# Optimization experiments

Measured on AMD Instinct MI355X. Metric: run time of the kernel, lower is better.

Reference implementation:

```python
import jax, jax.numpy as jnp
import numpy as np
import math

NQ = 6        # n_qubits_data
NL = 2        # n_layers (active_layers == n_layers)
K = 3         # unfold kernel
C = 64        # channels
SD = 128      # style_dim
B, H, W = 8, 64, 64
PD = C * K * K  # patch_dim = 576


def _apply_1q(psi, U, w):
    # psi: [bsz, 2,2,...,2]; U: [2,2] or [bsz,2,2]
    psi = jnp.moveaxis(psi, 1 + w, -1)
    if U.ndim == 2:
        psi = jnp.einsum('...j,ij->...i', psi, U)
    else:
        psi = jnp.einsum('b...j,bij->b...i', psi, U)
    return jnp.moveaxis(psi, -1, 1 + w)


def _ry_mat(theta):
    c = jnp.cos(theta / 2)
    s = jnp.sin(theta / 2)
    m = jnp.stack([jnp.stack([c, -s], -1), jnp.stack([s, c], -1)], -2)
    return m.astype(jnp.complex64)


def _rz_mat(theta):
    t = theta.astype(jnp.complex64)
    em = jnp.exp(-0.5j * t)
    ep = jnp.exp(0.5j * t)
    z = jnp.zeros_like(em)
    return jnp.stack([jnp.stack([em, z], -1), jnp.stack([z, ep], -1)], -2)


def _u3_mat(theta, phi, lam):
    t = theta.astype(jnp.complex64)
    p = phi.astype(jnp.complex64)
    l = lam.astype(jnp.complex64)
    ct = jnp.cos(t / 2)
    st = jnp.sin(t / 2)
    return jnp.stack([
        jnp.stack([ct, -jnp.exp(1j * l) * st], -1),
        jnp.stack([jnp.exp(1j * p) * st, jnp.exp(1j * (p + l)) * ct], -1)
    ], -2)


def _cnot(psi, c, t):
    c0, c1 = jnp.split(psi, 2, axis=1 + c)
    c1 = jnp.flip(c1, axis=1 + t)
    return jnp.concatenate([c0, c1], axis=1 + c)


def _forward(x, style, data_proj_w, data_proj_b, style_to_data_w, style_to_data_b,
             qcnn_rot_params, measure_params, out_proj_w, out_proj_b,
             res_proj_w, res_proj_b):
    Bx, Cx, Hx, Wx = x.shape
    # nn.Unfold(3, padding=1): [B, C*9, H*W], channel-major then kernel pos
    xp = jnp.pad(x, ((0, 0), (0, 0), (1, 1), (1, 1)))
    pats = jnp.stack([xp[:, :, i:i + Hx, j:j + Wx]
                      for i in range(K) for j in range(K)], axis=2)  # [B,C,9,H,W]
    patches_flat = pats.reshape(Bx, Cx * K * K, Hx * Wx).transpose(0, 2, 1).reshape(-1, Cx * K * K)
    style_flat = jnp.broadcast_to(style[:, None, :], (Bx, Hx * Wx, style.shape[-1])).reshape(-1, style.shape[-1])

    data_angles = jnp.tanh(patches_flat @ data_proj_w.T + data_proj_b) * math.pi   # [bsz, NQ]
    style_angles = jnp.tanh(style_flat @ style_to_data_w.T + style_to_data_b) * math.pi

    bsz = patches_flat.shape[0]
    psi = jnp.zeros((bsz,) + (2,) * NQ, jnp.complex64)
    psi = psi.at[(slice(None),) + (0,) * NQ].set(1.0)

    # hybrid encoding: RY(data + style) per wire (batched angles)
    theta0 = data_angles + style_angles
    for i in range(NQ):
        psi = _apply_1q(psi, _ry_mat(theta0[:, i]), i)

    # HEA layers: per-wire RY/RZ (scalar params) + ring CNOTs
    for l in range(NL):
        for i in range(NQ):
            psi = _apply_1q(psi, _ry_mat(qcnn_rot_params[l, i, 0, 0]), i)
            psi = _apply_1q(psi, _rz_mat(qcnn_rot_params[l, i, 1, 0]), i)
        for i in range(NQ):
            psi = _cnot(psi, i, (i + 1) % NQ)

    # trainable measurement basis (U3 per wire)
    for i in range(NQ):
        psi = _apply_1q(psi, _u3_mat(measure_params[i, 0], measure_params[i, 1], measure_params[i, 2]), i)

    # PauliZ expvals on all wires
    probs = psi.real ** 2 + psi.imag ** 2
    expvals = []
    for i in range(NQ):
        p = jnp.sum(probs, axis=tuple(a for a in range(1, NQ + 1) if a != 1 + i))  # [bsz,2]
        expvals.append(p[:, 0] - p[:, 1])
    quant_out = jnp.stack(expvals, -1)  # [bsz, NQ]

    out_flat = (quant_out @ out_proj_w.T + out_proj_b) + (patches_flat @ res_proj_w.T + res_proj_b)
    return out_flat.reshape(Bx, Hx, Wx, -1).transpose(0, 3, 1, 2)


def setup_inputs() -> dict:
    key = jax.random.key(0)
    ks = jax.random.split(key, 10)
    return {
        'x': jax.random.normal(ks[0], (B, C, H, W), jnp.float32),
        'style': jax.random.normal(ks[1], (B, SD), jnp.float32),
        'data_proj_w': jax.random.normal(ks[2], (NQ, PD), jnp.float32) * 0.02,
        'data_proj_b': jnp.zeros((NQ,), jnp.float32),
        'style_to_data_w': jax.random.normal(ks[3], (NQ, SD), jnp.float32) * 0.02,
        'style_to_data_b': jnp.zeros((NQ,), jnp.float32),
        'qcnn_rot_params': jax.random.normal(ks[4], (NL, NQ, 2, 3), jnp.float32) * 0.1,
        'measure_params': jax.random.normal(ks[5], (NQ, 3), jnp.float32) * 0.1,
        'out_proj_w': jax.random.normal(ks[6], (C, NQ), jnp.float32) * 0.02,
        'out_proj_b': jnp.zeros((C,), jnp.float32),
        'res_proj_w': jax.random.normal(ks[7], (C, PD), jnp.float32) * 0.02,
        'res_proj_b': jnp.zeros((C,), jnp.float32),
    }


def reference(x, style, data_proj_w, data_proj_b, style_to_data_w, style_to_data_b,
              qcnn_rot_params, measure_params, out_proj_w, out_proj_b,
              res_proj_w, res_proj_b):
    return _forward(x, style, data_proj_w, data_proj_b, style_to_data_w, style_to_data_b,
                    qcnn_rot_params, measure_params, out_proj_w, out_proj_b,
                    res_proj_w, res_proj_b)
```

## Files before the change

### kernel.cpp

```cpp
#include <hip/hip_runtime.h>
#include <math.h>

#define PI_F 3.14159265358979323846f

typedef __attribute__((ext_vector_type(8))) short bf16x8;
typedef __attribute__((ext_vector_type(4))) float f32x4;

__device__ float g_sang[48];
__device__ float g_cb[64];
__device__ __attribute__((aligned(16))) unsigned short g_Urb[64 * 64];
__device__ __attribute__((aligned(16))) unsigned short g_Uib[64 * 64];
__device__ __attribute__((aligned(16))) unsigned short g_Zwc[64 * 64];
__device__ __attribute__((aligned(16))) unsigned short g_Bm[5 * 18 * 64 * 8];

__device__ inline unsigned short bf16rne(float f) {
    unsigned u = __float_as_uint(f);
    return (unsigned short)((u + 0x7FFFu + ((u >> 16) & 1u)) >> 16);
}

__global__ __launch_bounds__(64) void k_prep(
        const float* __restrict__ style,
        const float* __restrict__ dw, const float* __restrict__ rw,
        const float* __restrict__ s2dw, const float* __restrict__ s2db,
        const float* __restrict__ qcnn, const float* __restrict__ meas,
        const float* __restrict__ outw, const float* __restrict__ outb,
        const float* __restrict__ resb) {
    int bid = blockIdx.x;
    int t = threadIdx.x;

    if (bid >= 66) {
        int entry = (bid - 66) * 64 + t;
        int nt   = entry / 1152;
        int rem  = entry - nt * 1152;
        int slab = rem >> 6;
        int ln   = rem & 63;
        int m    = ln & 15, quad = ln >> 4;
        int n    = nt * 16 + m;
        int ij   = slab >> 1;
        int ch   = (slab & 1) * 32;
#pragma unroll
        for (int j = 0; j < 8; ++j) {
            int c = ch + quad * 8 + j;
            int ko = c * 9 + ij;
            float v = 0.f;
            if (n < 64)      v = rw[n * 576 + ko];
            else if (n < 70) v = dw[(n - 64) * 576 + ko];
            g_Bm[entry * 8 + j] = bf16rne(v);
        }
        return;
    }
    if (bid == 0) {
        float zr[6];
#pragma unroll
        for (int q = 0; q < 6; ++q) zr[q] = ((t >> (5 - q)) & 1) ? -1.f : 1.f;
#pragma unroll 8
        for (int c = 0; c < 64; ++c) {
            float z = 0.f;
#pragma unroll
            for (int q = 0; q < 6; ++q) z += outw[c * 6 + q] * zr[q];
            g_Zwc[c * 64 + t] = bf16rne(z);
        }
        g_cb[t] = outb[t] + resb[t];
        return;
    }
    if (bid == 1) {
        if (t < 48) {
            int bb = t / 6, q = t % 6;
            float a = s2db[q];
#pragma unroll 8
            for (int j = 0; j < 128; ++j) a += style[bb * 128 + j] * s2dw[q * 128 + j];
            g_sang[t] = tanhf(a) * PI_F;
        }
        return;
    }

    int s = bid - 2;
    float ar = (t == s) ? 1.f : 0.f;
    float ai = 0.f;

#pragma unroll
    for (int l = 0; l < 2; ++l) {
#pragma unroll
        for (int wq = 0; wq < 6; ++wq) {
            int mask = 1 << (5 - wq);
            bool hi = (t & mask) != 0;
            float th = qcnn[((l * 6 + wq) * 2 + 0) * 3];
            float sg, cg; sincosf(0.5f * th, &sg, &cg);
            float pr = __shfl_xor(ar, mask);
            float pi2 = __shfl_xor(ai, mask);
            ar = hi ? (sg * pr + cg * ar) : (cg * ar - sg * pr);
            ai = hi ? (sg * pi2 + cg * ai) : (cg * ai - sg * pi2);
            float ph = qcnn[((l * 6 + wq) * 2 + 1) * 3];
            float sz, cz; sincosf(0.5f * ph, &sz, &cz);
            float szz = hi ? sz : -sz;
            float nr = cz * ar - szz * ai;
            float ni = cz * ai + szz * ar;
            ar = nr; ai = ni;
        }
#pragma unroll
        for (int wq = 0; wq < 6; ++wq) {
            int cm = 1 << (5 - wq);
            int tm = 1 << (5 - ((wq + 1) % 6));
            float pr = __shfl_xor(ar, tm);
            float pi2 = __shfl_xor(ai, tm);
            if (t & cm) { ar = pr; ai = pi2; }
        }
    }
#pragma unroll
    for (int wq = 0; wq < 6; ++wq) {
        int mask = 1 << (5 - wq);
        bool hi = (t & mask) != 0;
        float th = meas[wq * 3 + 0], ph = meas[wq * 3 + 1], lm = meas[wq * 3 + 2];
        float st2, ct; sincosf(0.5f * th, &st2, &ct);
        float sl, cl;  sincosf(lm, &sl, &cl);
        float sp, cp;  sincosf(ph, &sp, &cp);
        float spl, cpl; sincosf(ph + lm, &spl, &cpl);
        float u01r = -cl * st2, u01i = -sl * st2;
        float u10r =  cp * st2, u10i =  sp * st2;
        float u11r =  cpl * ct, u11i =  spl * ct;
        float pr = __shfl_xor(ar, mask);
        float pi2 = __shfl_xor(ai, mask);
        float nr, ni;
        if (hi) {
            nr = u10r * pr - u10i * pi2 + u11r * ar - u11i * ai;
            ni = u10r * pi2 + u10i * pr + u11r * ai + u11i * ar;
        } else {
            nr = ct * ar + u01r * pr - u01i * pi2;
            ni = ct * ai + u01r * pi2 + u01i * pr;
        }
        ar = nr; ai = ni;
    }
    g_Urb[t * 64 + s] = bf16rne(ar);
    g_Uib[t * 64 + s] = bf16rne(ai);
}

__global__ __launch_bounds__(1024, 4) void k_main(const float* __restrict__ x,
                                                  const float* __restrict__ dpb,
                                                  float* __restrict__ out) {
    __shared__ __attribute__((aligned(16))) float smem[13504];
    unsigned*             xsu32 = (unsigned*)smem;
    const unsigned short* xsu   = (const unsigned short*)smem;
    float*          convres = smem + 8320;
    float*          fact    = smem;
    unsigned short* psi_bf  = (unsigned short*)(smem + 1024);
    unsigned short* p_bf    = (unsigned short*)(smem + 3328);

    int tid  = threadIdx.x;
    int lane = tid & 63;
    int wid  = __builtin_amdgcn_readfirstlane(tid >> 6);
    int m    = lane & 15;
    int quad = lane >> 4;

    int p = blockIdx.x * 64 + lane;
    int b = p >> 12;
    int h = (p >> 6) & 63;
    int w = p & 63;
    const float* xb = x + (b << 18);

    if (tid < 216) {
        int r3 = tid / 72, rest = tid % 72;
        int half = rest / 36, cp = rest % 36;
        xsu32[(r3 * 66 + half * 65) * 36 + cp] = 0u;
    }
#pragma unroll
    for (int k = 0; k < 6; ++k) {
        int flat = k * 1024 + tid;
        int row  = flat >> 11;
        int rem  = flat & 2047;
        int cp   = rem >> 6;
        int w2   = rem & 63;
        int hh   = h + row - 1;
        float v0 = 0.f, v1 = 0.f;
        if ((unsigned)hh < 64u) {
            const float* px = xb + (hh << 6) + w2;
            v0 = px[(2 * cp) << 12];
            v1 = px[(2 * cp + 1) << 12];
        }
        xsu32[(row * 66 + w2 + 1) * 36 + cp] =
            (unsigned)bf16rne(v0) | ((unsigned)bf16rne(v1) << 16);
    }
    __syncthreads();

    int mt0 = wid >> 2, nt0 = wid & 3;
    const unsigned short* a0base = xsu + (mt0 * 16 + m) * 72 + quad * 8;
    const unsigned short* b0base = g_Bm + ((nt0 * 18) * 64 + lane) * 8;
    f32x4 acc0 = {0.f, 0.f, 0.f, 0.f};
    f32x4 acc1 = {0.f, 0.f, 0.f, 0.f};
    if (wid < 4) {
        const unsigned short* a1base = xsu + (wid * 16 + m) * 72 + quad * 8;
        const unsigned short* b1base = g_Bm + ((4 * 18) * 64 + lane) * 8;
#pragma unroll
        for (int slab = 0; slab < 18; ++slab) {
            int ij = slab >> 1, i = ij / 3, j = ij - 3 * (ij / 3);
            int aoff = i * 4752 + j * 72 + (slab & 1) * 32;
            bf16x8 a0 = *(const bf16x8*)(a0base + aoff);
            bf16x8 b0 = *(const bf16x8*)(b0base + slab * 512);
            acc0 = __builtin_amdgcn_mfma_f32_16x16x32_bf16(a0, b0, acc0, 0, 0, 0);
            bf16x8 a1 = *(const bf16x8*)(a1base + aoff);
            bf16x8 b1 = *(const bf16x8*)(b1base + slab * 512);
            acc1 = __builtin_amdgcn_mfma_f32_16x16x32_bf16(a1, b1, acc1, 0, 0, 0);
        }
    } else {
#pragma unroll
        for (int slab = 0; slab < 18; ++slab) {
            int ij = slab >> 1, i = ij / 3, j = ij - 3 * (ij / 3);
            int aoff = i * 4752 + j * 72 + (slab & 1) * 32;
            bf16x8 a0 = *(const bf16x8*)(a0base + aoff);
            bf16x8 b0 = *(const bf16x8*)(b0base + slab * 512);
            acc0 = __builtin_amdgcn_mfma_f32_16x16x32_bf16(a0, b0, acc0, 0, 0, 0);
        }
    }
#pragma unroll
    for (int r = 0; r < 4; ++r) {
        convres[(mt0 * 16 + quad * 4 + r) * 81 + nt0 * 16 + m] = acc0[r];
    }
    if (wid < 4) {
#pragma unroll
        for (int r = 0; r < 4; ++r) {
            convres[(wid * 16 + quad * 4 + r) * 81 + 64 + m] = acc1[r];
        }
    }
    __syncthreads();

    if (wid < 6) {
        int q = wid;
        float t = convres[lane * 81 + 64 + q];
        float theta = tanhf(t + dpb[q]) * PI_F + g_sang[b * 6 + q];
        float sv, cv; sincosf(0.5f * theta, &sv, &cv);
        fact[q * 64 + lane] = sv;
        fact[(6 + q) * 64 + lane] = cv;
    }
    __syncthreads();

    {
        float f0s = fact[0 * 64 + lane], f0c = fact[6 * 64 + lane];
        float f1s = fact[1 * 64 + lane], f1c = fact[7 * 64 + lane];
        float f2s = fact[2 * 64 + lane], f2c = fact[8 * 64 + lane];
        float f3s = fact[3 * 64 + lane], f3c = fact[9 * 64 + lane];
        float f4s = fact[4 * 64 + lane], f4c = fact[10 * 64 + lane];
        float f5s = fact[5 * 64 + lane], f5c = fact[11 * 64 + lane];
        int sb = wid * 4;
        float pre = (((sb >> 5) & 1) ? f0s : f0c)
                  * (((sb >> 4) & 1) ? f1s : f1c)
                  * (((sb >> 3) & 1) ? f2s : f2c)
                  * (((sb >> 2) & 1) ? f3s : f3c);
        unsigned short pk[4];
#pragma unroll
        for (int ti = 0; ti < 4; ++ti) {
            float v = pre * ((ti & 2) ? f4s : f4c) * ((ti & 1) ? f5s : f5c);
            pk[ti] = bf16rne(v);
        }
        *(uint2*)(psi_bf + lane * 72 + sb) =
            make_uint2((unsigned)pk[0] | ((unsigned)pk[1] << 16),
                       (unsigned)pk[2] | ((unsigned)pk[3] << 16));
    }
    __syncthreads();

    {
        const unsigned short* pa = psi_bf + (mt0 * 16 + m) * 72 + quad * 8;
        const unsigned short* ur = g_Urb + (nt0 * 16 + m) * 64 + quad * 8;
        const unsigned short* ui = g_Uib + (nt0 * 16 + m) * 64 + quad * 8;
        bf16x8 aA = *(const bf16x8*)(pa);
        bf16x8 aB = *(const bf16x8*)(pa + 32);
        f32x4 c1 = {0.f, 0.f, 0.f, 0.f};
        f32x4 c2 = {0.f, 0.f, 0.f, 0.f};
        c1 = __builtin_amdgcn_mfma_f32_16x16x32_bf16(aA, *(const bf16x8*)(ur), c1, 0, 0, 0);
        c1 = __builtin_amdgcn_mfma_f32_16x16x32_bf16(aB, *(const bf16x8*)(ur + 32), c1, 0, 0, 0);
        c2 = __builtin_amdgcn_mfma_f32_16x16x32_bf16(aA, *(const bf16x8*)(ui), c2, 0, 0, 0);
        c2 = __builtin_amdgcn_mfma_f32_16x16x32_bf16(aB, *(const bf16x8*)(ui + 32), c2, 0, 0, 0);
#pragma unroll
        for (int r = 0; r < 4; ++r) {
            float pv = c1[r] * c1[r] + c2[r] * c2[r];
            p_bf[(mt0 * 16 + quad * 4 + r) * 72 + nt0 * 16 + m] = bf16rne(pv);
        }
    }
    __syncthreads();

    {
        const unsigned short* pa = p_bf + (mt0 * 16 + m) * 72 + quad * 8;
        const unsigned short* zc = g_Zwc + (nt0 * 16 + m) * 64 + quad * 8;
        f32x4 o = {0.f, 0.f, 0.f, 0.f};
        o = __builtin_amdgcn_mfma_f32_16x16x32_bf16(*(const bf16x8*)(pa),
                                                    *(const bf16x8*)(zc), o, 0, 0, 0);
        o = __builtin_amdgcn_mfma_f32_16x16x32_bf16(*(const bf16x8*)(pa + 32),
                                                    *(const bf16x8*)(zc + 32), o, 0, 0, 0);
#pragma unroll
        for (int r = 0; r < 4; ++r) {
            convres[(mt0 * 16 + quad * 4 + r) * 81 + nt0 * 16 + m] += o[r];
        }
    }
    __syncthreads();

    int ob = (b << 18) + (h << 6) + w;
#pragma unroll
    for (int kk = 0; kk < 4; ++kk) {
        int c = wid * 4 + kk;
        out[ob + (c << 12)] = convres[lane * 81 + c] + g_cb[c];
    }
}

extern "C" void kernel_launch(void* const* d_in, const int* in_sizes, int n_in,
                              void* d_out, int out_size, void* d_ws, size_t ws_size,
                              hipStream_t stream) {
    const float* x     = (const float*)d_in[0];
    const float* style = (const float*)d_in[1];
    const float* dw    = (const float*)d_in[2];
    const float* dpb   = (const float*)d_in[3];
    const float* s2dw  = (const float*)d_in[4];
    const float* s2db  = (const float*)d_in[5];
    const float* qcnn  = (const float*)d_in[6];
    const float* meas  = (const float*)d_in[7];
    const float* outw  = (const float*)d_in[8];
    const float* outb  = (const float*)d_in[9];
    const float* rw    = (const float*)d_in[10];
    const float* resb  = (const float*)d_in[11];
    float* out = (float*)d_out;

    hipLaunchKernelGGL(k_prep, dim3(156), dim3(64), 0, stream,
                       style, dw, rw, s2dw, s2db, qcnn, meas, outw, outb, resb);
    hipLaunchKernelGGL(k_main, dim3(512), dim3(1024), 0, stream, x, dpb, out);
}
```

Measured before the change: 108.8 us.

## Fuse weight-prep kernel into main kernel, recomputing constants per block in LDS

Removes the separate prep kernel launch and instead has every block of the main kernel rebuild the bf16 weight tiles, circuit unitary, Z-weight matrix and style angles directly into shared memory. This drops one launch and the global round-trip for the prepared constants. In exchange, each of the 512 blocks redundantly reads about 40K weights, converts them, and runs the quantum circuit simulation. Shared memory grows from about 54KB to about 156KB per block, which likely limits occupancy to one block per CU.

```diff
diff --git a/kernel.cpp b/kernel.cpp
--- a/kernel.cpp
+++ b/kernel.cpp
@@ -5,145 +5,47 @@
 
 typedef __attribute__((ext_vector_type(8))) short bf16x8;
 typedef __attribute__((ext_vector_type(4))) float f32x4;
-
-__device__ float g_sang[48];
-__device__ float g_cb[64];
-__device__ __attribute__((aligned(16))) unsigned short g_Urb[64 * 64];
-__device__ __attribute__((aligned(16))) unsigned short g_Uib[64 * 64];
-__device__ __attribute__((aligned(16))) unsigned short g_Zwc[64 * 64];
-__device__ __attribute__((aligned(16))) unsigned short g_Bm[5 * 18 * 64 * 8];
 
 __device__ inline unsigned short bf16rne(float f) {
     unsigned u = __float_as_uint(f);
     return (unsigned short)((u + 0x7FFFu + ((u >> 16) & 1u)) >> 16);
 }
 
-__global__ __launch_bounds__(64) void k_prep(
-        const float* __restrict__ style,
-        const float* __restrict__ dw, const float* __restrict__ rw,
-        const float* __restrict__ s2dw, const float* __restrict__ s2db,
-        const float* __restrict__ qcnn, const float* __restrict__ meas,
-        const float* __restrict__ outw, const float* __restrict__ outb,
-        const float* __restrict__ resb) {
-    int bid = blockIdx.x;
-    int t = threadIdx.x;
-
-    if (bid >= 66) {
-        int entry = (bid - 66) * 64 + t;
-        int nt   = entry / 1152;
-        int rem  = entry - nt * 1152;
-        int slab = rem >> 6;
-        int ln   = rem & 63;
-        int m    = ln & 15, quad = ln >> 4;
-        int n    = nt * 16 + m;
-        int ij   = slab >> 1;
-        int ch   = (slab & 1) * 32;
-#pragma unroll
-        for (int j = 0; j < 8; ++j) {
-            int c = ch + quad * 8 + j;
-            int ko = c * 9 + ij;
-            float v = 0.f;
-            if (n < 64)      v = rw[n * 576 + ko];
-            else if (n < 70) v = dw[(n - 64) * 576 + ko];
-            g_Bm[entry * 8 + j] = bf16rne(v);
-        }
-        return;
-    }
-    if (bid == 0) {
-        float zr[6];
-#pragma unroll
-        for (int q = 0; q < 6; ++q) zr[q] = ((t >> (5 - q)) & 1) ? -1.f : 1.f;
-#pragma unroll 8
-        for (int c = 0; c < 64; ++c) {
-            float z = 0.f;
-#pragma unroll
-            for (int q = 0; q < 6; ++q) z += outw[c * 6 + q] * zr[q];
-            g_Zwc[c * 64 + t] = bf16rne(z);
-        }
-        g_cb[t] = outb[t] + resb[t];
-        return;
-    }
-    if (bid == 1) {
-        if (t < 48) {
-            int bb = t / 6, q = t % 6;
-            float a = s2db[q];
-#pragma unroll 8
-            for (int j = 0; j < 128; ++j) a += style[bb * 128 + j] * s2dw[q * 128 + j];
-            g_sang[t] = tanhf(a) * PI_F;
-        }
-        return;
-    }
-
-    int s = bid - 2;
-    float ar = (t == s) ? 1.f : 0.f;
-    float ai = 0.f;
-
-#pragma unroll
-    for (int l = 0; l < 2; ++l) {
-#pragma unroll
-        for (int wq = 0; wq < 6; ++wq) {
-            int mask = 1 << (5 - wq);
-            bool hi = (t & mask) != 0;
-            float th = qcnn[((l * 6 + wq) * 2 + 0) * 3];
-            float sg, cg; sincosf(0.5f * th, &sg, &cg);
-            float pr = __shfl_xor(ar, mask);
-            float pi2 = __shfl_xor(ai, mask);
-            ar = hi ? (sg * pr + cg * ar) : (cg * ar - sg * pr);
-            ai = hi ? (sg * pi2 + cg * ai) : (cg * ai - sg * pi2);
-            float ph = qcnn[((l * 6 + wq) * 2 + 1) * 3];
-            float sz, cz; sincosf(0.5f * ph, &sz, &cz);
-            float szz = hi ? sz : -sz;
-            float nr = cz * ar - szz * ai;
-            float ni = cz * ai + szz * ar;
-            ar = nr; ai = ni;
-        }
-#pragma unroll
-        for (int wq = 0; wq < 6; ++wq) {
-            int cm = 1 << (5 - wq);
-            int tm = 1 << (5 - ((wq + 1) % 6));
-            float pr = __shfl_xor(ar, tm);
-            float pi2 = __shfl_xor(ai, tm);
-            if (t & cm) { ar = pr; ai = pi2; }
-        }
-    }
-#pragma unroll
-    for (int wq = 0; wq < 6; ++wq) {
-        int mask = 1 << (5 - wq);
-        bool hi = (t & mask) != 0;
-        float th = meas[wq * 3 + 0], ph = meas[wq * 3 + 1], lm = meas[wq * 3 + 2];
-        float st2, ct; sincosf(0.5f * th, &st2, &ct);
-        float sl, cl;  sincosf(lm, &sl, &cl);
-        float sp, cp;  sincosf(ph, &sp, &cp);
-        float spl, cpl; sincosf(ph + lm, &spl, &cpl);
-        float u01r = -cl * st2, u01i = -sl * st2;
-        float u10r =  cp * st2, u10i =  sp * st2;
-        float u11r =  cpl * ct, u11i =  spl * ct;
-        float pr = __shfl_xor(ar, mask);
-        float pi2 = __shfl_xor(ai, mask);
-        float nr, ni;
-        if (hi) {
-            nr = u10r * pr - u10i * pi2 + u11r * ar - u11i * ai;
-            ni = u10r * pi2 + u10i * pr + u11r * ai + u11i * ar;
-        } else {
-            nr = ct * ar + u01r * pr - u01i * pi2;
-            ni = ct * ai + u01r * pi2 + u01i * pr;
-        }
-        ar = nr; ai = ni;
-    }
-    g_Urb[t * 64 + s] = bf16rne(ar);
-    g_Uib[t * 64 + s] = bf16rne(ai);
-}
-
-__global__ __launch_bounds__(1024, 4) void k_main(const float* __restrict__ x,
-                                                  const float* __restrict__ dpb,
-                                                  float* __restrict__ out) {
-    __shared__ __attribute__((aligned(16))) float smem[13504];
+#define XS_OFF    0
+#define FACT_OFF  0
+#define PSI_OFF   1024
+#define PBF_OFF   3328
+#define CR_OFF    8320
+#define BM_OFF    13504
+#define URB_OFF   31936
+#define UIB_OFF   34240
+#define ZWC_OFF   36544
+#define SANG_OFF  38848
+#define CB_OFF    38896
+#define SMEM_FLOATS 38960
+
+__global__ __launch_bounds__(1024, 4) void k_all(
+        const float* __restrict__ x,     const float* __restrict__ style,
+        const float* __restrict__ dw,    const float* __restrict__ dpb,
+        const float* __restrict__ s2dw,  const float* __restrict__ s2db,
+        const float* __restrict__ qcnn,  const float* __restrict__ meas,
+        const float* __restrict__ outw,  const float* __restrict__ outb,
+        const float* __restrict__ rw,    const float* __restrict__ resb,
+        float* __restrict__ out) {
+    __shared__ __attribute__((aligned(16))) float smem[SMEM_FLOATS];
     unsigned*             xsu32 = (unsigned*)smem;
     const unsigned short* xsu   = (const unsigned short*)smem;
-    float*          convres = smem + 8320;
-    float*          fact    = smem;
-    unsigned short* psi_bf  = (unsigned short*)(smem + 1024);
-    unsigned short* p_bf    = (unsigned short*)(smem + 3328);
+    float*          convres = smem + CR_OFF;
+    float*          fact    = smem + FACT_OFF;
+    unsigned short* psi_bf  = (unsigned short*)(smem + PSI_OFF);
+    unsigned short* p_bf    = (unsigned short*)(smem + PBF_OFF);
+    unsigned short* BmU     = (unsigned short*)(smem + BM_OFF);
+    unsigned short* Bm4U    = (unsigned short*)(smem + CR_OFF);
+    unsigned short* Ur      = (unsigned short*)(smem + URB_OFF);
+    unsigned short* Ui      = (unsigned short*)(smem + UIB_OFF);
+    unsigned short* Zwc     = (unsigned short*)(smem + ZWC_OFF);
+    float* s_sang = smem + SANG_OFF;
+    float* s_cb   = smem + CB_OFF;
 
     int tid  = threadIdx.x;
     int lane = tid & 63;
@@ -162,6 +64,13 @@
         int half = rest / 36, cp = rest % 36;
         xsu32[(r3 * 66 + half * 65) * 36 + cp] = 0u;
     }
+    if (tid < 720) {
+        int slab = tid / 40, r2 = tid % 40;
+        int q4 = r2 / 10, mm = 6 + (r2 % 10);
+        uint4 z = {0u, 0u, 0u, 0u};
+        *(uint4*)(Bm4U + ((slab * 64 + (q4 << 4) + mm) << 3)) = z;
+    }
+
 #pragma unroll
     for (int k = 0; k < 6; ++k) {
         int flat = k * 1024 + tid;
@@ -179,16 +88,136 @@
         xsu32[(row * 66 + w2 + 1) * 36 + cp] =
             (unsigned)bf16rne(v0) | ((unsigned)bf16rne(v1) << 16);
     }
+
+#pragma unroll 4
+    for (int it = 0; it < 40; ++it) {
+        int flat = it * 1024 + tid;
+        if (flat < 40320) {
+            int n = flat / 576;
+            int k = flat - n * 576;
+            float v = (n < 64) ? rw[flat] : dw[flat - 36864];
+            int c  = k / 9;
+            int ij = k - 9 * c;
+            int slab = (ij << 1) | (c >> 5);
+            int ln   = (((c >> 3) & 3) << 4) | (n & 15);
+            int j    = c & 7;
+            unsigned short* dst = (n < 64)
+                ? (BmU  + (((n >> 4) * 1152 + slab * 64 + ln) << 3) + j)
+                : (Bm4U + ((slab * 64 + ln) << 3) + j);
+            *dst = bf16rne(v);
+        }
+    }
+
+    {
+        int s0 = wid * 4;
+        float ar[4], ai[4];
+#pragma unroll
+        for (int cc = 0; cc < 4; ++cc) {
+            ar[cc] = (lane == s0 + cc) ? 1.f : 0.f;
+            ai[cc] = 0.f;
+        }
+#pragma unroll
+        for (int l = 0; l < 2; ++l) {
+#pragma unroll
+            for (int wq = 0; wq < 6; ++wq) {
+                int mask = 1 << (5 - wq);
+                bool hi = (lane & mask) != 0;
+                float th = qcnn[((l * 6 + wq) * 2 + 0) * 3];
+                float sg, cg; sincosf(0.5f * th, &sg, &cg);
+                float ph = qcnn[((l * 6 + wq) * 2 + 1) * 3];
+                float sz, cz; sincosf(0.5f * ph, &sz, &cz);
+                float szz = hi ? sz : -sz;
+#pragma unroll
+                for (int cc = 0; cc < 4; ++cc) {
+                    float pr  = __shfl_xor(ar[cc], mask);
+                    float pi2 = __shfl_xor(ai[cc], mask);
+                    float nr = hi ? (sg * pr + cg * ar[cc]) : (cg * ar[cc] - sg * pr);
+                    float ni = hi ? (sg * pi2 + cg * ai[cc]) : (cg * ai[cc] - sg * pi2);
+                    ar[cc] = cz * nr - szz * ni;
+                    ai[cc] = cz * ni + szz * nr;
+                }
+            }
+#pragma unroll
+            for (int wq = 0; wq < 6; ++wq) {
+                int cm = 1 << (5 - wq);
+                int tm = 1 << (5 - ((wq + 1) % 6));
+#pragma unroll
+                for (int cc = 0; cc < 4; ++cc) {
+                    float pr  = __shfl_xor(ar[cc], tm);
+                    float pi2 = __shfl_xor(ai[cc], tm);
+                    if (lane & cm) { ar[cc] = pr; ai[cc] = pi2; }
+                }
+            }
+        }
+#pragma unroll
+        for (int wq = 0; wq < 6; ++wq) {
+            int mask = 1 << (5 - wq);
+            bool hi = (lane & mask) != 0;
+            float th = meas[wq * 3 + 0], ph = meas[wq * 3 + 1], lm = meas[wq * 3 + 2];
+            float st2, ct; sincosf(0.5f * th, &st2, &ct);
+            float sl, cl;  sincosf(lm, &sl, &cl);
+            float sp, cp;  sincosf(ph, &sp, &cp);
+            float spl, cpl; sincosf(ph + lm, &spl, &cpl);
+            float u01r = -cl * st2, u01i = -sl * st2;
+            float u10r =  cp * st2, u10i =  sp * st2;
+            float u11r =  cpl * ct, u11i =  spl * ct;
+#pragma unroll
+            for (int cc = 0; cc < 4; ++cc) {
+                float pr  = __shfl_xor(ar[cc], mask);
+                float pi2 = __shfl_xor(ai[cc], mask);
+                float nr, ni;
+                if (hi) {
+                    nr = u10r * pr - u10i * pi2 + u11r * ar[cc] - u11i * ai[cc];
+                    ni = u10r * pi2 + u10i * pr + u11r * ai[cc] + u11i * ar[cc];
+                } else {
+                    nr = ct * ar[cc] + u01r * pr - u01i * pi2;
+                    ni = ct * ai[cc] + u01r * pi2 + u01i * pr;
+                }
+                ar[cc] = nr; ai[cc] = ni;
+            }
+        }
+        unsigned short rr[4], ii[4];
+#pragma unroll
+        for (int cc = 0; cc < 4; ++cc) { rr[cc] = bf16rne(ar[cc]); ii[cc] = bf16rne(ai[cc]); }
+        uint2 pr_ = make_uint2((unsigned)rr[0] | ((unsigned)rr[1] << 16),
+                               (unsigned)rr[2] | ((unsigned)rr[3] << 16));
+        uint2 pi_ = make_uint2((unsigned)ii[0] | ((unsigned)ii[1] << 16),
+                               (unsigned)ii[2] | ((unsigned)ii[3] << 16));
+        *(uint2*)(Ur + lane * 72 + s0) = pr_;
+        *(uint2*)(Ui + lane * 72 + s0) = pi_;
+    }
+
+    {
+        float zr[6];
+#pragma unroll
+        for (int q = 0; q < 6; ++q) zr[q] = ((lane >> (5 - q)) & 1) ? -1.f : 1.f;
+#pragma unroll
+        for (int cc = 0; cc < 4; ++cc) {
+            int c = wid * 4 + cc;
+            float z = 0.f;
+#pragma unroll
+            for (int q = 0; q < 6; ++q) z += outw[c * 6 + q] * zr[q];
+            Zwc[c * 72 + lane] = bf16rne(z);
+        }
+    }
+    if (wid == 6) s_cb[lane] = outb[lane] + resb[lane];
+    if (wid == 7 && lane < 48) {
+        int bb = lane / 6, q = lane % 6;
+        float a = s2db[q];
+#pragma unroll 8
+        for (int j = 0; j < 128; ++j) a += style[bb * 128 + j] * s2dw[q * 128 + j];
+        s_sang[lane] = tanhf(a) * PI_F;
+    }
     __syncthreads();
 
     int mt0 = wid >> 2, nt0 = wid & 3;
     const unsigned short* a0base = xsu + (mt0 * 16 + m) * 72 + quad * 8;
-    const unsigned short* b0base = g_Bm + ((nt0 * 18) * 64 + lane) * 8;
+    const unsigned short* b0base = BmU + (nt0 * 1152 + lane) * 8;
     f32x4 acc0 = {0.f, 0.f, 0.f, 0.f};
     f32x4 acc1 = {0.f, 0.f, 0.f, 0.f};
     if (wid < 4) {
         const unsigned short* a1base = xsu + (wid * 16 + m) * 72 + quad * 8;
-        const unsigned short* b1base = g_Bm + ((4 * 18) * 64 + lane) * 8;
+        const unsigned short* b1base = Bm4U + lane * 8;
 #pragma unroll
         for (int slab = 0; slab < 18; ++slab) {
             int ij = slab >> 1, i = ij / 3, j = ij - 3 * (ij / 3);
@@ -210,6 +239,7 @@
             acc0 = __builtin_amdgcn_mfma_f32_16x16x32_bf16(a0, b0, acc0, 0, 0, 0);
         }
     }
+    __syncthreads();
 #pragma unroll
     for (int r = 0; r < 4; ++r) {
         convres[(mt0 * 16 + quad * 4 + r) * 81 + nt0 * 16 + m] = acc0[r];
@@ -225,7 +255,7 @@
     if (wid < 6) {
         int q = wid;
         float t = convres[lane * 81 + 64 + q];
-        float theta = tanhf(t + dpb[q]) * PI_F + g_sang[b * 6 + q];
+        float theta = tanhf(t + dpb[q]) * PI_F + s_sang[b * 6 + q];
         float sv, cv; sincosf(0.5f * theta, &sv, &cv);
         fact[q * 64 + lane] = sv;
         fact[(6 + q) * 64 + lane] = cv;
@@ -258,8 +288,8 @@
 
     {
         const unsigned short* pa = psi_bf + (mt0 * 16 + m) * 72 + quad * 8;
-        const unsigned short* ur = g_Urb + (nt0 * 16 + m) * 64 + quad * 8;
-        const unsigned short* ui = g_Uib + (nt0 * 16 + m) * 64 + quad * 8;
+        const unsigned short* ur = Ur + (nt0 * 16 + m) * 72 + quad * 8;
+        const unsigned short* ui = Ui + (nt0 * 16 + m) * 72 + quad * 8;
         bf16x8 aA = *(const bf16x8*)(pa);
         bf16x8 aB = *(const bf16x8*)(pa + 32);
         f32x4 c1 = {0.f, 0.f, 0.f, 0.f};
@@ -278,7 +308,7 @@
 
     {
         const unsigned short* pa = p_bf + (mt0 * 16 + m) * 72 + quad * 8;
-        const unsigned short* zc = g_Zwc + (nt0 * 16 + m) * 64 + quad * 8;
+        const unsigned short* zc = Zwc + (nt0 * 16 + m) * 72 + quad * 8;
         f32x4 o = {0.f, 0.f, 0.f, 0.f};
         o = __builtin_amdgcn_mfma_f32_16x16x32_bf16(*(const bf16x8*)(pa),
                                                     *(const bf16x8*)(zc), o, 0, 0, 0);
@@ -295,7 +325,7 @@
 #pragma unroll
     for (int kk = 0; kk < 4; ++kk) {
         int c = wid * 4 + kk;
-        out[ob + (c << 12)] = convres[lane * 81 + c] + g_cb[c];
+        out[ob + (c << 12)] = convres[lane * 81 + c] + s_cb[c];
     }
 }
 
@@ -316,7 +346,7 @@
     const float* resb  = (const float*)d_in[11];
     float* out = (float*)d_out;
 
-    hipLaunchKernelGGL(k_prep, dim3(156), dim3(64), 0, stream,
-                       style, dw, rw, s2dw, s2db, qcnn, meas, outw, outb, resb);
-    hipLaunchKernelGGL(k_main, dim3(512), dim3(1024), 0, stream, x, dpb, out);
+    hipLaunchKernelGGL(k_all, dim3(512), dim3(1024), 0, stream,
+                       x, style, dw, dpb, s2dw, s2db, qcnn, meas,
+                       outw, outb, rw, resb, out);
 }
```

Result: slower. 152.3 us (+40.1%).
